# Kernel optimization log

Hardware: AMD Instinct MI355X
Metric: run time of the kernel (lower is better)

Reference implementation:

```python
import jax, jax.numpy as jnp
import numpy as np

N_HEADS = 8
OUT_FEATURES = 64
LEAKY_SLOPE = 0.2
MASK_FILL = -1e9


def setup_inputs() -> dict:
    key = jax.random.key(0)
    k_h, k_adj, k_W, k_a = jax.random.split(key, 4)
    B, N, F_IN = 1, 4096, 128
    h = jax.random.normal(k_h, (B, N, F_IN), dtype=jnp.float32)
    adj_mat = jax.random.randint(k_adj, (N, N), 0, 2, dtype=jnp.int32)
    # glorot-style scaled params
    W = jax.random.normal(k_W, (F_IN, OUT_FEATURES * N_HEADS), dtype=jnp.float32) * (1.0 / np.sqrt(F_IN))
    a = jax.random.normal(k_a, (N_HEADS, 2 * OUT_FEATURES, 1), dtype=jnp.float32) * (1.0 / np.sqrt(2 * OUT_FEATURES))
    return {"h": h, "adj_mat": adj_mat, "W": W, "a": a}


def reference(h, adj_mat, W, a):
    B, N, _ = h.shape
    heads = a.shape[0]
    out = a.shape[1] // 2
    # linear transform + head split (same reshape order as tf.reshape)
    ht = jnp.reshape(h @ W, (-1, heads, N, out))            # (B, heads, N, out)
    # additive attention scores
    src = jnp.einsum('bhnf,hfo->bhno', ht, a[:, :out, :])    # (B, heads, N, 1)
    tgt = jnp.einsum('bhnf,hfo->bhno', ht, a[:, out:, :])    # (B, heads, N, 1)
    e = src + jnp.swapaxes(tgt, -1, -2)                      # (B, heads, N, N)
    e = jnp.where(e > 0, e, LEAKY_SLOPE * e)                 # leaky_relu
    e = jnp.where(adj_mat > 0, e, MASK_FILL)                 # adjacency mask
    attention = jax.nn.softmax(e, axis=-1)
    h_prime = attention @ ht                                 # (B, heads, N, out)
    return h_prime
```

## Files before the change

### kernel.cpp

```cpp
#include <hip/hip_runtime.h>
#include <stdint.h>

#define HT_STRIDE 262144
#define LOG2E 1.4426950408889634f

typedef __attribute__((ext_vector_type(8))) short bf16x8;
typedef __attribute__((ext_vector_type(4))) float f32x4;
typedef __attribute__((ext_vector_type(2))) float f32x2;

__device__ __forceinline__ unsigned short f2bf(float f) {
    unsigned int u = __float_as_uint(f);
    u += 0x7FFFu + ((u >> 16) & 1u);
    return (unsigned short)(u >> 16);
}

__device__ __forceinline__ float exp2_fast(float e) {
#if __has_builtin(__builtin_amdgcn_exp2f)
    return __builtin_amdgcn_exp2f(e);
#else
    return __expf(e * 0.6931471805599453f);
#endif
}

__global__ void __launch_bounds__(256) k_fused(const float* __restrict__ h,
                                               const int* __restrict__ adj,
                                               const float* __restrict__ W,
                                               const float* __restrict__ aW,
                                               float* __restrict__ src,
                                               float* __restrict__ tgt,
                                               unsigned short* __restrict__ htT2,
                                               unsigned int* __restrict__ abm) {
    __shared__ unsigned int ldsT[1024];
    __shared__ float hs[8][128];
    __shared__ float ldsA[64][66];
    __shared__ float redS[4][64];
    __shared__ float redT[4][64];
    const int t = threadIdx.x;

    if (blockIdx.x < 512) {
        const int lane = t & 63;
        const int w = t >> 6;
        const int sb = blockIdx.x >> 3;
        const int cq = blockIdx.x & 7;
        for (int rr = 0; rr < 16; ++rr) {
            const int* arow = adj + (sb * 64 + w * 16 + rr) * 4096 + cq * 512;
            int v[8];
            #pragma unroll
            for (int j = 0; j < 8; ++j) v[j] = arow[j * 64 + lane];
            #pragma unroll
            for (int j = 0; j < 8; ++j) {
                unsigned long long m = __ballot(v[j] > 0);
                if (lane < 2)
                    ldsT[(2 * j + lane) * 64 + rr * 4 + w] = (unsigned int)(m >> (lane * 32));
            }
        }
        __syncthreads();
        ((uint4*)(abm + (sb * 128 + cq * 16) * 64))[t] = ((uint4*)ldsT)[t];
    } else {
        const int bid2 = (int)blockIdx.x - 512;
        const int n0 = bid2 * 8;
        const int p0 = bid2 * 64;
        const int hd = p0 >> 12;
        const int m0 = p0 & 4095;

        {
            float4 v = ((const float4*)(h + n0 * 128))[t];
            int e = t * 4;
            int r = e >> 7, f = e & 127;
            hs[r][f + 0] = v.x; hs[r][f + 1] = v.y;
            hs[r][f + 2] = v.z; hs[r][f + 3] = v.w;
        }
        __syncthreads();

        float acc0[8], acc1[8];
        #pragma unroll
        for (int r = 0; r < 8; ++r) { acc0[r] = 0.f; acc1[r] = 0.f; }
        const float2* Wf = (const float2*)W;
        for (int f = 0; f < 128; ++f) {
            float2 wp = Wf[f * 256 + t];
            #pragma unroll
            for (int r = 0; r < 8; ++r) {
                float hv = hs[r][f];
                acc0[r] = fmaf(hv, wp.x, acc0[r]);
                acc1[r] = fmaf(hv, wp.y, acc1[r]);
            }
        }
        {
            const int ns = t >> 5;
            const int o = (2 * t) & 63;
            #pragma unroll
            for (int r = 0; r < 8; ++r) {
                *(float2*)&ldsA[r * 8 + ns][o] = make_float2(acc0[r], acc1[r]);
            }
        }
        __syncthreads();

        {
            const int r = t & 63, og = t >> 6;
            float sdot = 0.f, gdot = 0.f;
            #pragma unroll
            for (int k = 0; k < 16; ++k) {
                int o = og * 16 + k;
                float hv = ldsA[r][o];
                sdot = fmaf(hv, aW[hd * 128 + o], sdot);
                gdot = fmaf(hv, aW[hd * 128 + 64 + o], gdot);
            }
            redS[og][r] = sdot; redT[og][r] = gdot;
        }
        __syncthreads();
        if (t < 64) {
            src[p0 + t] = (redS[0][t] + redS[1][t] + redS[2][t] + redS[3][t]) * LOG2E;
        } else if (t < 128) {
            int r = t - 64;
            tgt[p0 + r] = (redT[0][r] + redT[1][r] + redT[2][r] + redT[3][r]) * LOG2E;
        }

        unsigned short* d = htT2 + (hd * 128 + (m0 >> 5)) * 2048;
        #pragma unroll
        for (int i = 0; i < 16; ++i) {
            int id = t + 256 * i;
            int mi = id & 31, o = (id >> 5) & 63, ct = id >> 11;
            d[ct * 2048 + o * 32 + mi] = f2bf(ldsA[mi + 32 * ct][o]);
        }
    }
}

__global__ void __launch_bounds__(256, 4) k_attn(const unsigned int* __restrict__ abm,
                                                 const unsigned short* __restrict__ htT2,
                                                 const float* __restrict__ srcv,
                                                 const float* __restrict__ tgtv,
                                                 float* __restrict__ out) {
    __shared__ __align__(16) float smem[8192];
    float* tgl = smem;
    uint2* bm2 = (uint2*)(smem + 4096);

    const int t = threadIdx.x;
    const int kq = t >> 6;
    const int lane = t & 63;
    const int li = lane & 15;
    const int quad = lane >> 4;
    const int head = blockIdx.x & 7;
    const int s32 = blockIdx.x >> 3;
    const int s64 = s32 >> 1, half = s32 & 1;
    const int i0 = s32 * 32;

    {
        const float4* tsrc = (const float4*)(tgtv + head * 4096);
        float4* tdst = (float4*)tgl;
        #pragma unroll
        for (int i = 0; i < 4; ++i) tdst[t + 256 * i] = tsrc[t + 256 * i];

        const unsigned int* base = abm + s64 * 8192 + half * 2;
        #pragma unroll
        for (int i = 0; i < 8; ++i) {
            int p = t + 256 * i;
            int c = p >> 4, lw = p & 15;
            bm2[p] = *(const uint2*)(base + c * 64 + lw * 4);
        }
    }

    f32x2 a2[2], b2[2];
    #pragma unroll
    for (int g2 = 0; g2 < 2; ++g2) {
        float sv = srcv[head * 4096 + i0 + 16 * g2 + li];
        a2[g2] = (f32x2){sv, sv};
        b2[g2] = (f32x2){0.2f * sv, 0.2f * sv};
    }

    f32x4 acc[8];
    #pragma unroll
    for (int i = 0; i < 8; ++i) acc[i] = (f32x4){0.f, 0.f, 0.f, 0.f};
    f32x4 apd[2];
    apd[0] = (f32x4){0.f, 0.f, 0.f, 0.f};
    apd[1] = (f32x4){0.f, 0.f, 0.f, 0.f};

    const uint4 onesw = {0x3F803F80u, 0x3F803F80u, 0x3F803F80u, 0x3F803F80u};
    const bf16x8 aones = __builtin_bit_cast(bf16x8, onesw);

    const uint4* ap = (const uint4*)(htT2 + head * HT_STRIDE) + (li * 4 + quad);

    __syncthreads();

    const int c0 = kq * 32;
    uint4 avb[2][4];
    #pragma unroll
    for (int f = 0; f < 4; ++f) avb[0][f] = ap[c0 * 256 + f * 64];

    #pragma unroll 2
    for (int ci = 0; ci < 32; ++ci) {
        const int cur = ci & 1;
        const int c = c0 + ci;
        const int cn = c0 + ((ci + 1) & 31);
        #pragma unroll
        for (int f = 0; f < 4; ++f) avb[cur ^ 1][f] = ap[cn * 256 + f * 64];

        const float* tk = tgl + c * 32 + quad * 8;
        float4 tg0 = ((const float4*)tk)[0];
        float4 tg1 = ((const float4*)tk)[1];
        uint2 bw = bm2[c * 16 + li];

        const float tt[8] = {tg0.x, tg0.y, tg0.z, tg0.w, tg1.x, tg1.y, tg1.z, tg1.w};
        const unsigned int wb[2] = {bw.x, bw.y};
        #pragma unroll
        for (int g2 = 0; g2 < 2; ++g2) {
            const unsigned int wq = wb[g2] >> (quad * 8);
            unsigned int pk[4];
            #pragma unroll
            for (int m = 0; m < 4; ++m) {
                f32x2 tp = (f32x2){tt[2 * m], tt[2 * m + 1]};
                f32x2 t1 = tp + a2[g2];
                f32x2 t2 = tp * 0.2f + b2[g2];
                float p0e = exp2_fast(fmaxf(t1[0], t2[0]));
                float p1e = exp2_fast(fmaxf(t1[1], t2[1]));
                float w0 = (wq & (1u << (2 * m)))     ? p0e : 0.f;
                float w1 = (wq & (1u << (2 * m + 1))) ? p1e : 0.f;
                asm("v_cvt_pk_bf16_f32 %0, %1, %2" : "=v"(pk[m]) : "v"(w0), "v"(w1));
            }
            uint4 bv; bv.x = pk[0]; bv.y = pk[1]; bv.z = pk[2]; bv.w = pk[3];
            bf16x8 bfrag = __builtin_bit_cast(bf16x8, bv);
            apd[g2] = __builtin_amdgcn_mfma_f32_16x16x32_bf16(aones, bfrag, apd[g2], 0, 0, 0);
            acc[g2 * 4 + 0] = __builtin_amdgcn_mfma_f32_16x16x32_bf16(__builtin_bit_cast(bf16x8, avb[cur][0]), bfrag, acc[g2 * 4 + 0], 0, 0, 0);
            acc[g2 * 4 + 1] = __builtin_amdgcn_mfma_f32_16x16x32_bf16(__builtin_bit_cast(bf16x8, avb[cur][1]), bfrag, acc[g2 * 4 + 1], 0, 0, 0);
            acc[g2 * 4 + 2] = __builtin_amdgcn_mfma_f32_16x16x32_bf16(__builtin_bit_cast(bf16x8, avb[cur][2]), bfrag, acc[g2 * 4 + 2], 0, 0, 0);
            acc[g2 * 4 + 3] = __builtin_amdgcn_mfma_f32_16x16x32_bf16(__builtin_bit_cast(bf16x8, avb[cur][3]), bfrag, acc[g2 * 4 + 3], 0, 0, 0);
        }
    }

    __syncthreads();
    if (kq != 0) {
        float* cb = smem + ((kq - 1) * 64 + lane) * 36;
        #pragma unroll
        for (int i = 0; i < 8; ++i) ((f32x4*)cb)[i] = acc[i];
        cb[32] = apd[0][0]; cb[33] = apd[1][0];
    }
    __syncthreads();
    if (kq == 0) {
        float pd[2] = {apd[0][0], apd[1][0]};
        #pragma unroll
        for (int q = 0; q < 3; ++q) {
            const float* cb = smem + (q * 64 + lane) * 36;
            #pragma unroll
            for (int i = 0; i < 8; ++i) acc[i] += ((const f32x4*)cb)[i];
            pd[0] += cb[32]; pd[1] += cb[33];
        }
        #pragma unroll
        for (int g2 = 0; g2 < 2; ++g2) {
            const float rd = 1.0f / pd[g2];
            float4* op = (float4*)(out + head * HT_STRIDE + (i0 + 16 * g2 + li) * 64);
            #pragma unroll
            for (int f = 0; f < 4; ++f) {
                f32x4 a = acc[g2 * 4 + f];
                op[f * 4 + quad] = make_float4(a[0] * rd, a[1] * rd, a[2] * rd, a[3] * rd);
            }
        }
    }
}

extern "C" void kernel_launch(void* const* d_in, const int* in_sizes, int n_in,
                              void* d_out, int out_size, void* d_ws, size_t ws_size,
                              hipStream_t stream) {
    const float* h   = (const float*)d_in[0];
    const int*   adj = (const int*)d_in[1];
    const float* W   = (const float*)d_in[2];
    const float* aW  = (const float*)d_in[3];
    float* out = (float*)d_out;

    char* ws = (char*)d_ws;
    float* src  = (float*)(ws);
    float* tgt  = (float*)(ws + 131072);
    unsigned int*   abm  = (unsigned int*)(ws + 262144);
    unsigned short* htT2 = (unsigned short*)(ws + 2359296);

    hipLaunchKernelGGL(k_fused, dim3(1024), dim3(256), 0, stream,
                       h, adj, W, aW, src, tgt, htT2, abm);
    hipLaunchKernelGGL(k_attn,  dim3(1024), dim3(256), 0, stream,
                       abm, htT2, src, tgt, out);
}
```

Before: 155.5 us.

## Factor exponentials into precomputed per-node terms and drop LDS staging of bitmask

The exponential of the leaky-relu score is factored as exp2(s)*exp2(t) or exp2(0.2s)*exp2(0.2t), with the branch chosen by comparing exp2(t) against exp2(-s). The producer kernel now stores both target exponentials, and the attention kernel computes only the source ones, so the inner loop does a multiply instead of two exp2 per element. The adjacency bitmask is read straight from global memory instead of being staged in LDS, masking is done with bitwise ANDs on the packed bf16 values, and the register double-buffering of the value fragments is removed with the loop left unrolled by one. Risks are possible overflow or underflow of the factored exponentials, extra load latency now that there is no prefetch, and uncached bitmask reads.

```diff
diff --git a/kernel.cpp b/kernel.cpp
--- a/kernel.cpp
+++ b/kernel.cpp
@@ -26,8 +26,8 @@
                                                const int* __restrict__ adj,
                                                const float* __restrict__ W,
                                                const float* __restrict__ aW,
-                                               float* __restrict__ src,
-                                               float* __restrict__ tgt,
+                                               float* __restrict__ srcv,
+                                               float* __restrict__ ets,
                                                unsigned short* __restrict__ htT2,
                                                unsigned int* __restrict__ abm) {
     __shared__ unsigned int ldsT[1024];
@@ -109,10 +109,12 @@
         }
         __syncthreads();
         if (t < 64) {
-            src[p0 + t] = (redS[0][t] + redS[1][t] + redS[2][t] + redS[3][t]) * LOG2E;
+            srcv[p0 + t] = (redS[0][t] + redS[1][t] + redS[2][t] + redS[3][t]) * LOG2E;
         } else if (t < 128) {
             int r = t - 64;
-            tgt[p0 + r] = (redT[0][r] + redT[1][r] + redT[2][r] + redT[3][r]) * LOG2E;
+            float tv = (redT[0][r] + redT[1][r] + redT[2][r] + redT[3][r]) * LOG2E;
+            ets[(p0 + r) * 2 + 0] = exp2_fast(tv);
+            ets[(p0 + r) * 2 + 1] = exp2_fast(0.2f * tv);
         }
 
         unsigned short* d = htT2 + (hd * 128 + (m0 >> 5)) * 2048;
@@ -128,11 +130,9 @@
 __global__ void __launch_bounds__(256, 4) k_attn(const unsigned int* __restrict__ abm,
                                                  const unsigned short* __restrict__ htT2,
                                                  const float* __restrict__ srcv,
-                                                 const float* __restrict__ tgtv,
+                                                 const float* __restrict__ ets,
                                                  float* __restrict__ out) {
     __shared__ __align__(16) float smem[8192];
-    float* tgl = smem;
-    uint2* bm2 = (uint2*)(smem + 4096);
 
     const int t = threadIdx.x;
     const int kq = t >> 6;
@@ -145,26 +145,19 @@
     const int i0 = s32 * 32;
 
     {
-        const float4* tsrc = (const float4*)(tgtv + head * 4096);
-        float4* tdst = (float4*)tgl;
-        #pragma unroll
-        for (int i = 0; i < 4; ++i) tdst[t + 256 * i] = tsrc[t + 256 * i];
-
-        const unsigned int* base = abm + s64 * 8192 + half * 2;
-        #pragma unroll
-        for (int i = 0; i < 8; ++i) {
-            int p = t + 256 * i;
-            int c = p >> 4, lw = p & 15;
-            bm2[p] = *(const uint2*)(base + c * 64 + lw * 4);
-        }
-    }
-
-    f32x2 a2[2], b2[2];
+        const float4* esrc = (const float4*)(ets + head * 8192);
+        float4* edst = (float4*)smem;
+        #pragma unroll
+        for (int i = 0; i < 8; ++i) edst[t + 256 * i] = esrc[t + 256 * i];
+    }
+
+    float es[2], es2[2], eth[2];
     #pragma unroll
     for (int g2 = 0; g2 < 2; ++g2) {
-        float sv = srcv[head * 4096 + i0 + 16 * g2 + li];
-        a2[g2] = (f32x2){sv, sv};
-        b2[g2] = (f32x2){0.2f * sv, 0.2f * sv};
+        float sp = srcv[head * 4096 + i0 + 16 * g2 + li];
+        es[g2]  = exp2_fast(sp);
+        es2[g2] = exp2_fast(0.2f * sp);
+        eth[g2] = exp2_fast(-sp);
     }
 
     f32x4 acc[8];
@@ -178,28 +171,25 @@
     const bf16x8 aones = __builtin_bit_cast(bf16x8, onesw);
 
     const uint4* ap = (const uint4*)(htT2 + head * HT_STRIDE) + (li * 4 + quad);
+    const unsigned int* bmp = abm + s64 * 8192 + half * 2 + li * 4;
 
     __syncthreads();
 
     const int c0 = kq * 32;
-    uint4 avb[2][4];
-    #pragma unroll
-    for (int f = 0; f < 4; ++f) avb[0][f] = ap[c0 * 256 + f * 64];
-
-    #pragma unroll 2
+    #pragma unroll 1
     for (int ci = 0; ci < 32; ++ci) {
-        const int cur = ci & 1;
         const int c = c0 + ci;
-        const int cn = c0 + ((ci + 1) & 31);
-        #pragma unroll
-        for (int f = 0; f < 4; ++f) avb[cur ^ 1][f] = ap[cn * 256 + f * 64];
-
-        const float* tk = tgl + c * 32 + quad * 8;
-        float4 tg0 = ((const float4*)tk)[0];
-        float4 tg1 = ((const float4*)tk)[1];
-        uint2 bw = bm2[c * 16 + li];
-
-        const float tt[8] = {tg0.x, tg0.y, tg0.z, tg0.w, tg1.x, tg1.y, tg1.z, tg1.w};
+        uint4 av0 = ap[c * 256 + 0];
+        uint4 av1 = ap[c * 256 + 64];
+        uint4 av2 = ap[c * 256 + 128];
+        uint4 av3 = ap[c * 256 + 192];
+        uint2 bw = *(const uint2*)(bmp + c * 64);
+
+        const float4* ep = (const float4*)(smem + c * 64 + quad * 16);
+        float4 e0 = ep[0], e1 = ep[1], e2 = ep[2], e3 = ep[3];
+        const float etv[8]  = {e0.x, e0.z, e1.x, e1.z, e2.x, e2.z, e3.x, e3.z};
+        const float et2v[8] = {e0.y, e0.w, e1.y, e1.w, e2.y, e2.w, e3.y, e3.w};
+
         const unsigned int wb[2] = {bw.x, bw.y};
         #pragma unroll
         for (int g2 = 0; g2 < 2; ++g2) {
@@ -207,22 +197,29 @@
             unsigned int pk[4];
             #pragma unroll
             for (int m = 0; m < 4; ++m) {
-                f32x2 tp = (f32x2){tt[2 * m], tt[2 * m + 1]};
-                f32x2 t1 = tp + a2[g2];
-                f32x2 t2 = tp * 0.2f + b2[g2];
-                float p0e = exp2_fast(fmaxf(t1[0], t2[0]));
-                float p1e = exp2_fast(fmaxf(t1[1], t2[1]));
-                float w0 = (wq & (1u << (2 * m)))     ? p0e : 0.f;
-                float w1 = (wq & (1u << (2 * m + 1))) ? p1e : 0.f;
-                asm("v_cvt_pk_bf16_f32 %0, %1, %2" : "=v"(pk[m]) : "v"(w0), "v"(w1));
+                const int j0 = 2 * m, j1 = 2 * m + 1;
+                const bool cb0 = etv[j0] > eth[g2];
+                const bool cb1 = etv[j1] > eth[g2];
+                f32x2 ee, ss;
+                ee[0] = cb0 ? etv[j0] : et2v[j0];
+                ee[1] = cb1 ? etv[j1] : et2v[j1];
+                ss[0] = cb0 ? es[g2] : es2[g2];
+                ss[1] = cb1 ? es[g2] : es2[g2];
+                f32x2 ww = ee * ss;
+                unsigned int pkm;
+                asm("v_cvt_pk_bf16_f32 %0, %1, %2" : "=v"(pkm) : "v"(ww[0]), "v"(ww[1]));
+                const unsigned int lo = (unsigned int)((int)(wq << (31 - j0)) >> 31);
+                const unsigned int hi = (unsigned int)((int)(wq << (31 - j1)) >> 31);
+                const unsigned int msk = (lo & 0x0000FFFFu) | (hi & 0xFFFF0000u);
+                pk[m] = pkm & msk;
             }
             uint4 bv; bv.x = pk[0]; bv.y = pk[1]; bv.z = pk[2]; bv.w = pk[3];
             bf16x8 bfrag = __builtin_bit_cast(bf16x8, bv);
             apd[g2] = __builtin_amdgcn_mfma_f32_16x16x32_bf16(aones, bfrag, apd[g2], 0, 0, 0);
-            acc[g2 * 4 + 0] = __builtin_amdgcn_mfma_f32_16x16x32_bf16(__builtin_bit_cast(bf16x8, avb[cur][0]), bfrag, acc[g2 * 4 + 0], 0, 0, 0);
-            acc[g2 * 4 + 1] = __builtin_amdgcn_mfma_f32_16x16x32_bf16(__builtin_bit_cast(bf16x8, avb[cur][1]), bfrag, acc[g2 * 4 + 1], 0, 0, 0);
-            acc[g2 * 4 + 2] = __builtin_amdgcn_mfma_f32_16x16x32_bf16(__builtin_bit_cast(bf16x8, avb[cur][2]), bfrag, acc[g2 * 4 + 2], 0, 0, 0);
-            acc[g2 * 4 + 3] = __builtin_amdgcn_mfma_f32_16x16x32_bf16(__builtin_bit_cast(bf16x8, avb[cur][3]), bfrag, acc[g2 * 4 + 3], 0, 0, 0);
+            acc[g2 * 4 + 0] = __builtin_amdgcn_mfma_f32_16x16x32_bf16(__builtin_bit_cast(bf16x8, av0), bfrag, acc[g2 * 4 + 0], 0, 0, 0);
+            acc[g2 * 4 + 1] = __builtin_amdgcn_mfma_f32_16x16x32_bf16(__builtin_bit_cast(bf16x8, av1), bfrag, acc[g2 * 4 + 1], 0, 0, 0);
+            acc[g2 * 4 + 2] = __builtin_amdgcn_mfma_f32_16x16x32_bf16(__builtin_bit_cast(bf16x8, av2), bfrag, acc[g2 * 4 + 2], 0, 0, 0);
+            acc[g2 * 4 + 3] = __builtin_amdgcn_mfma_f32_16x16x32_bf16(__builtin_bit_cast(bf16x8, av3), bfrag, acc[g2 * 4 + 3], 0, 0, 0);
         }
     }
 
@@ -266,13 +263,13 @@
     float* out = (float*)d_out;
 
     char* ws = (char*)d_ws;
-    float* src  = (float*)(ws);
-    float* tgt  = (float*)(ws + 131072);
-    unsigned int*   abm  = (unsigned int*)(ws + 262144);
-    unsigned short* htT2 = (unsigned short*)(ws + 2359296);
+    float* srcv = (float*)(ws);
+    float* ets  = (float*)(ws + 131072);
+    unsigned int*   abm  = (unsigned int*)(ws + 393216);
+    unsigned short* htT2 = (unsigned short*)(ws + 2490368);
 
     hipLaunchKernelGGL(k_fused, dim3(1024), dim3(256), 0, stream,
-                       h, adj, W, aW, src, tgt, htT2, abm);
+                       h, adj, W, aW, srcv, ets, htT2, abm);
     hipLaunchKernelGGL(k_attn,  dim3(1024), dim3(256), 0, stream,
-                       abm, htT2, src, tgt, out);
-}
+                       abm, htT2, srcv, ets, out);
+}
```

Result: faster. 150.8 us (-3.0%).
